# Kernel tuning notes

Measured on AMD Instinct MI355X. Metric: run time of the kernel, lower is better.

The kernel has to match this reference:

```python
import jax, jax.numpy as jnp
import numpy as np

B, T, I, H1, H2, OUT = 4096, 256, 2, 16, 64, 8


def _gru_layer(x, w_ih, w_hh, b_ih, b_hh):
    """PyTorch-semantics single-layer GRU. x: [T,B,I]. Returns (outputs [T,B,H], h_last [B,H]).
    Gate order is r,z,n as in torch.nn.GRU."""
    H = w_hh.shape[1]
    # precompute input projections for all timesteps (one big GEMM)
    gx_all = jnp.einsum('tbi,gi->tbg', x, w_ih) + b_ih  # [T,B,3H]

    def step(h, gx):
        gh = h @ w_hh.T + b_hh  # [B,3H]
        xr, xz, xn = jnp.split(gx, 3, axis=-1)
        hr, hz, hn = jnp.split(gh, 3, axis=-1)
        r = jax.nn.sigmoid(xr + hr)
        z = jax.nn.sigmoid(xz + hz)
        n = jnp.tanh(xn + r * hn)
        h_new = (1.0 - z) * n + z * h
        return h_new, h_new

    h0 = jnp.zeros((x.shape[1], H), dtype=x.dtype)
    h_last, out = jax.lax.scan(step, h0, gx_all)
    return out, h_last


def setup_inputs() -> dict:
    key = jax.random.key(0)
    ks = jax.random.split(key, 10)
    s = 0.3  # keep gates out of saturation, mimics orthogonal-ish scale
    return {
        'all_traj': jax.random.normal(ks[0], (B, T, I), jnp.float32),
        'w_ih1': s * jax.random.normal(ks[1], (3 * H1, I), jnp.float32),
        'w_hh1': s * jax.random.normal(ks[2], (3 * H1, H1), jnp.float32),
        'b_ih1': jnp.zeros((3 * H1,), jnp.float32),
        'b_hh1': jnp.zeros((3 * H1,), jnp.float32),
        'w_ih2f': s * jax.random.normal(ks[3], (3 * H2, H1), jnp.float32),
        'w_hh2f': s * jax.random.normal(ks[4], (3 * H2, H2), jnp.float32),
        'b_ih2f': jnp.zeros((3 * H2,), jnp.float32),
        'b_hh2f': jnp.zeros((3 * H2,), jnp.float32),
        'w_ih2b': s * jax.random.normal(ks[5], (3 * H2, H1), jnp.float32),
        'w_hh2b': s * jax.random.normal(ks[6], (3 * H2, H2), jnp.float32),
        'b_ih2b': jnp.zeros((3 * H2,), jnp.float32),
        'b_hh2b': jnp.zeros((3 * H2,), jnp.float32),
        'W1': 0.01 * jax.random.normal(ks[7], (32, H2), jnp.float32),
        'b1': jnp.zeros((32,), jnp.float32),
        'W2': 0.01 * jax.random.normal(ks[8], (OUT, 32), jnp.float32),
        'b2': jnp.zeros((OUT,), jnp.float32),
    }


def reference(all_traj, w_ih1, w_hh1, b_ih1, b_hh1,
              w_ih2f, w_hh2f, b_ih2f, b_hh2f,
              w_ih2b, w_hh2b, b_ih2b, b_hh2b,
              W1, b1, W2, b2):
    x = jnp.transpose(all_traj, (1, 0, 2))  # [T,B,I], matches torch.transpose(all_traj,0,1)
    out1, _ = _gru_layer(x, w_ih1, w_hh1, b_ih1, b_hh1)  # [T,B,16]
    # bidirectional layer: forward pass + reversed-time pass
    _, h_fwd = _gru_layer(out1, w_ih2f, w_hh2f, b_ih2f, b_hh2f)          # [B,64]
    _, h_bwd = _gru_layer(out1[::-1], w_ih2b, w_hh2b, b_ih2b, b_hh2b)    # [B,64]
    h = h_fwd + h_bwd  # torch.sum(h, 0) over the 2 directions -> [B,64]
    z = (h @ W1.T + b1) @ W2.T + b2  # MLP with no activation, as in source
    return z
```

## Files before the change

kernel.cpp:

```cpp
#include <hip/hip_runtime.h>

#define TT 256
#define BB 4096
#define EPB 4

__device__ __forceinline__ float sigm(float x) {
  float e = __expf(-x);
  return __builtin_amdgcn_rcpf(1.0f + e);
}

__device__ __forceinline__ float tanhx(float x) {
  x = fminf(15.0f, fmaxf(-15.0f, x));
  float e = __expf(-2.0f * x);
  return (1.0f - e) * __builtin_amdgcn_rcpf(1.0f + e);
}

#define DOT4(acc, wv, xv)                 \
  do {                                    \
    acc = fmaf((wv).x, (xv).x, acc);      \
    acc = fmaf((wv).y, (xv).y, acc);      \
    acc = fmaf((wv).z, (xv).z, acc);      \
    acc = fmaf((wv).w, (xv).w, acc);      \
  } while (0)

__global__ __launch_bounds__(128, 1) void gru_fused(
    const float* __restrict__ xin,
    const float* __restrict__ wih1,
    const float* __restrict__ whh1,
    const float* __restrict__ bih1,
    const float* __restrict__ bhh1,
    const float* __restrict__ wihf,
    const float* __restrict__ whhf,
    const float* __restrict__ bihf,
    const float* __restrict__ bhhf,
    const float* __restrict__ wihb,
    const float* __restrict__ whhb,
    const float* __restrict__ bihb,
    const float* __restrict__ bhhb,
    const float* __restrict__ W1,
    const float* __restrict__ b1,
    const float* __restrict__ W2,
    const float* __restrict__ b2,
    float* __restrict__ zout)
{
  __shared__ __align__(16) float out1L[EPB][TT][16];
  __shared__ __align__(16) float hs[2][EPB][64];
  __shared__ __align__(16) float hl1[EPB][16];
  __shared__ __align__(16) float ys[EPB][32];

  const int tid = threadIdx.x;
  const int w   = tid >> 6;
  const int l   = tid & 63;
  const int b0  = blockIdx.x * EPB;

  if (l < 32) {
    const int g = l >> 4;
    const int u = l & 15;
    const int e = w * 2 + g;

    float wr[16], wz[16], wn[16];
#pragma unroll
    for (int j = 0; j < 16; ++j) {
      wr[j] = whh1[u * 16 + j];
      wz[j] = whh1[(16 + u) * 16 + j];
      wn[j] = whh1[(32 + u) * 16 + j];
    }
    const float wir0 = wih1[2 * u],        wir1 = wih1[2 * u + 1];
    const float wiz0 = wih1[2 * (16 + u)], wiz1 = wih1[2 * (16 + u) + 1];
    const float win0 = wih1[2 * (32 + u)], win1 = wih1[2 * (32 + u) + 1];
    const float br  = bih1[u] + bhh1[u];
    const float bz  = bih1[16 + u] + bhh1[16 + u];
    const float bin = bih1[32 + u];
    const float bhn = bhh1[32 + u];

    const float2* xp = (const float2*)xin + (size_t)(b0 + e) * TT;

    float h = 0.0f;
    hl1[e][u] = 0.0f;
    for (int t = 0; t < TT; ++t) {
      float2 xv = xp[t];
      float ar = fmaf(wir1, xv.y, fmaf(wir0, xv.x, br));
      float az = fmaf(wiz1, xv.y, fmaf(wiz0, xv.x, bz));
      float an = fmaf(win1, xv.y, fmaf(win0, xv.x, bin));
      float hr = 0.f, hz = 0.f, hn = bhn;
#pragma unroll
      for (int j = 0; j < 16; ++j) {
        float hj = hl1[e][j];
        hr = fmaf(wr[j], hj, hr);
        hz = fmaf(wz[j], hj, hz);
        hn = fmaf(wn[j], hj, hn);
      }
      float r = sigm(ar + hr);
      float z = sigm(az + hz);
      float n = tanhx(fmaf(r, hn, an));
      h = fmaf(z, h - n, n);
      hl1[e][u] = h;
      out1L[e][t][u] = h;
    }
  }
  __syncthreads();

  const float* wih = w ? wihb : wihf;
  const float* whh = w ? whhb : whhf;
  const float* bih = w ? bihb : bihf;
  const float* bhh = w ? bhhb : bhhf;

  float4 wr2[16], wz2[16], wn2[16];
  {
    const float4* whh4 = (const float4*)whh;
#pragma unroll
    for (int j4 = 0; j4 < 16; ++j4) {
      wr2[j4] = whh4[l * 16 + j4];
      wz2[j4] = whh4[(64 + l) * 16 + j4];
      wn2[j4] = whh4[(128 + l) * 16 + j4];
    }
  }
  float4 wir2[4], wiz2[4], win2[4];
  {
    const float4* wih4 = (const float4*)wih;
#pragma unroll
    for (int i4 = 0; i4 < 4; ++i4) {
      wir2[i4] = wih4[l * 4 + i4];
      wiz2[i4] = wih4[(64 + l) * 4 + i4];
      win2[i4] = wih4[(128 + l) * 4 + i4];
    }
  }
  const float br2  = bih[l] + bhh[l];
  const float bz2  = bih[64 + l] + bhh[64 + l];
  const float bin2 = bih[128 + l];
  const float bhn2 = bhh[128 + l];

  float h0 = 0.f, h1 = 0.f, h2 = 0.f, h3 = 0.f;
  hs[w][0][l] = 0.f; hs[w][1][l] = 0.f; hs[w][2][l] = 0.f; hs[w][3][l] = 0.f;

#pragma unroll 1
  for (int t = 0; t < TT; ++t) {
    const int te = w ? (TT - 1 - t) : t;
    const float4* x0p = (const float4*)&out1L[0][te][0];
    const float4* x1p = (const float4*)&out1L[1][te][0];
    const float4* x2p = (const float4*)&out1L[2][te][0];
    const float4* x3p = (const float4*)&out1L[3][te][0];

    float ar0 = br2, az0 = bz2, an0 = bin2;
    float ar1 = br2, az1 = bz2, an1 = bin2;
    float ar2 = br2, az2 = bz2, an2 = bin2;
    float ar3 = br2, az3 = bz2, an3 = bin2;
#pragma unroll
    for (int i4 = 0; i4 < 4; ++i4) {
      const float4 wrv = wir2[i4], wzv = wiz2[i4], wnv = win2[i4];
      const float4 xa = x0p[i4], xb = x1p[i4], xc = x2p[i4], xd = x3p[i4];
      DOT4(ar0, wrv, xa); DOT4(az0, wzv, xa); DOT4(an0, wnv, xa);
      DOT4(ar1, wrv, xb); DOT4(az1, wzv, xb); DOT4(an1, wnv, xb);
      DOT4(ar2, wrv, xc); DOT4(az2, wzv, xc); DOT4(an2, wnv, xc);
      DOT4(ar3, wrv, xd); DOT4(az3, wzv, xd); DOT4(an3, wnv, xd);
    }

    float hr0 = 0.f, hz0 = 0.f, hn0 = bhn2;
    float hr1 = 0.f, hz1 = 0.f, hn1 = bhn2;
    float hr2 = 0.f, hz2 = 0.f, hn2 = bhn2;
    float hr3 = 0.f, hz3 = 0.f, hn3 = bhn2;
#pragma unroll
    for (int j4 = 0; j4 < 16; ++j4) {
      const float4 ha = *(const float4*)&hs[w][0][j4 * 4];
      const float4 hb = *(const float4*)&hs[w][1][j4 * 4];
      const float4 hc = *(const float4*)&hs[w][2][j4 * 4];
      const float4 hd = *(const float4*)&hs[w][3][j4 * 4];
      const float4 wrv = wr2[j4], wzv = wz2[j4], wnv = wn2[j4];
      DOT4(hr0, wrv, ha); DOT4(hz0, wzv, ha); DOT4(hn0, wnv, ha);
      DOT4(hr1, wrv, hb); DOT4(hz1, wzv, hb); DOT4(hn1, wnv, hb);
      DOT4(hr2, wrv, hc); DOT4(hz2, wzv, hc); DOT4(hn2, wnv, hc);
      DOT4(hr3, wrv, hd); DOT4(hz3, wzv, hd); DOT4(hn3, wnv, hd);
    }

    { float r = sigm(ar0 + hr0), z = sigm(az0 + hz0);
      float n = tanhx(fmaf(r, hn0, an0)); h0 = fmaf(z, h0 - n, n); }
    { float r = sigm(ar1 + hr1), z = sigm(az1 + hz1);
      float n = tanhx(fmaf(r, hn1, an1)); h1 = fmaf(z, h1 - n, n); }
    { float r = sigm(ar2 + hr2), z = sigm(az2 + hz2);
      float n = tanhx(fmaf(r, hn2, an2)); h2 = fmaf(z, h2 - n, n); }
    { float r = sigm(ar3 + hr3), z = sigm(az3 + hz3);
      float n = tanhx(fmaf(r, hn3, an3)); h3 = fmaf(z, h3 - n, n); }

    hs[w][0][l] = h0; hs[w][1][l] = h1; hs[w][2][l] = h2; hs[w][3][l] = h3;
  }
  __syncthreads();

  const int e3 = w * 2 + (l >> 5);
  const int s  = l & 31;
  const int bo = b0 + e3;
  {
    float acc = b1[s];
    const float4* w1r = (const float4*)(W1 + s * 64);
#pragma unroll
    for (int j4 = 0; j4 < 16; ++j4) {
      const float4 hv0 = *(const float4*)&hs[0][e3][j4 * 4];
      const float4 hv1 = *(const float4*)&hs[1][e3][j4 * 4];
      const float4 wv  = w1r[j4];
      acc = fmaf(wv.x, hv0.x + hv1.x, acc);
      acc = fmaf(wv.y, hv0.y + hv1.y, acc);
      acc = fmaf(wv.z, hv0.z + hv1.z, acc);
      acc = fmaf(wv.w, hv0.w + hv1.w, acc);
    }
    ys[e3][s] = acc;
  }
  if (s < 8) {
    float acc = b2[s];
#pragma unroll
    for (int j4 = 0; j4 < 8; ++j4) {
      const float4 yv = *(const float4*)&ys[e3][j4 * 4];
      const float4 wv = *(const float4*)&W2[s * 32 + j4 * 4];
      DOT4(acc, wv, yv);
    }
    zout[bo * 8 + s] = acc;
  }
}

extern "C" void kernel_launch(void* const* d_in, const int* in_sizes, int n_in,
                              void* d_out, int out_size, void* d_ws, size_t ws_size,
                              hipStream_t stream) {
  const float* all_traj = (const float*)d_in[0];
  const float* w_ih1  = (const float*)d_in[1];
  const float* w_hh1  = (const float*)d_in[2];
  const float* b_ih1  = (const float*)d_in[3];
  const float* b_hh1  = (const float*)d_in[4];
  const float* w_ih2f = (const float*)d_in[5];
  const float* w_hh2f = (const float*)d_in[6];
  const float* b_ih2f = (const float*)d_in[7];
  const float* b_hh2f = (const float*)d_in[8];
  const float* w_ih2b = (const float*)d_in[9];
  const float* w_hh2b = (const float*)d_in[10];
  const float* b_ih2b = (const float*)d_in[11];
  const float* b_hh2b = (const float*)d_in[12];
  const float* W1 = (const float*)d_in[13];
  const float* b1 = (const float*)d_in[14];
  const float* W2 = (const float*)d_in[15];
  const float* b2 = (const float*)d_in[16];
  float* z = (float*)d_out;

  gru_fused<<<BB / EPB, 128, 0, stream>>>(
      all_traj, w_ih1, w_hh1, b_ih1, b_hh1,
      w_ih2f, w_hh2f, b_ih2f, b_hh2f,
      w_ih2b, w_hh2b, b_ih2b, b_hh2b,
      W1, b1, W2, b2, z);
}
```

Before: 1.455 ms.

## Assign one batch element per wave per direction in bidirectional GRU layer

```diff
diff --git a/kernel.cpp b/kernel.cpp
--- a/kernel.cpp
+++ b/kernel.cpp
@@ -2,7 +2,7 @@
 
 #define TT 256
 #define BB 4096
-#define EPB 4
+#define EPB 2
 
 __device__ __forceinline__ float sigm(float x) {
   float e = __expf(-x);
@@ -23,7 +23,7 @@
     acc = fmaf((wv).w, (xv).w, acc);      \
   } while (0)
 
-__global__ __launch_bounds__(128, 1) void gru_fused(
+__global__ __launch_bounds__(256, 2) void gru_fused(
     const float* __restrict__ xin,
     const float* __restrict__ wih1,
     const float* __restrict__ whh1,
@@ -44,19 +44,20 @@
     float* __restrict__ zout)
 {
   __shared__ __align__(16) float out1L[EPB][TT][16];
-  __shared__ __align__(16) float hs[2][EPB][64];
+  __shared__ __align__(16) float hs[4][64];
   __shared__ __align__(16) float hl1[EPB][16];
   __shared__ __align__(16) float ys[EPB][32];
 
   const int tid = threadIdx.x;
   const int w   = tid >> 6;
   const int l   = tid & 63;
+  const int dir = w >> 1;
+  const int e   = w & 1;
   const int b0  = blockIdx.x * EPB;
 
-  if (l < 32) {
-    const int g = l >> 4;
-    const int u = l & 15;
-    const int e = w * 2 + g;
+  if (w < 2 && l < 16) {
+    const int u  = l;
+    const int e1 = w;
 
     float wr[16], wz[16], wn[16];
 #pragma unroll
@@ -73,10 +74,10 @@
     const float bin = bih1[32 + u];
     const float bhn = bhh1[32 + u];
 
-    const float2* xp = (const float2*)xin + (size_t)(b0 + e) * TT;
+    const float2* xp = (const float2*)xin + (size_t)(b0 + e1) * TT;
 
     float h = 0.0f;
-    hl1[e][u] = 0.0f;
+    hl1[e1][u] = 0.0f;
     for (int t = 0; t < TT; ++t) {
       float2 xv = xp[t];
       float ar = fmaf(wir1, xv.y, fmaf(wir0, xv.x, br));
@@ -85,7 +86,7 @@
       float hr = 0.f, hz = 0.f, hn = bhn;
 #pragma unroll
       for (int j = 0; j < 16; ++j) {
-        float hj = hl1[e][j];
+        float hj = hl1[e1][j];
         hr = fmaf(wr[j], hj, hr);
         hz = fmaf(wz[j], hj, hz);
         hn = fmaf(wn[j], hj, hn);
@@ -94,16 +95,16 @@
       float z = sigm(az + hz);
       float n = tanhx(fmaf(r, hn, an));
       h = fmaf(z, h - n, n);
-      hl1[e][u] = h;
-      out1L[e][t][u] = h;
+      hl1[e1][u] = h;
+      out1L[e1][t][u] = h;
     }
   }
   __syncthreads();
 
-  const float* wih = w ? wihb : wihf;
-  const float* whh = w ? whhb : whhf;
-  const float* bih = w ? bihb : bihf;
-  const float* bhh = w ? bhhb : bhhf;
+  const float* wih = dir ? wihb : wihf;
+  const float* whh = dir ? whhb : whhf;
+  const float* bih = dir ? bihb : bihf;
+  const float* bhh = dir ? bhhb : bhhf;
 
   float4 wr2[16], wz2[16], wn2[16];
   {
@@ -115,103 +116,90 @@
       wn2[j4] = whh4[(128 + l) * 16 + j4];
     }
   }
-  float4 wir2[4], wiz2[4], win2[4];
-  {
-    const float4* wih4 = (const float4*)wih;
-#pragma unroll
-    for (int i4 = 0; i4 < 4; ++i4) {
-      wir2[i4] = wih4[l * 4 + i4];
-      wiz2[i4] = wih4[(64 + l) * 4 + i4];
-      win2[i4] = wih4[(128 + l) * 4 + i4];
-    }
-  }
   const float br2  = bih[l] + bhh[l];
   const float bz2  = bih[64 + l] + bhh[64 + l];
   const float bin2 = bih[128 + l];
   const float bhn2 = bhh[128 + l];
 
-  float h0 = 0.f, h1 = 0.f, h2 = 0.f, h3 = 0.f;
-  hs[w][0][l] = 0.f; hs[w][1][l] = 0.f; hs[w][2][l] = 0.f; hs[w][3][l] = 0.f;
-
-#pragma unroll 1
-  for (int t = 0; t < TT; ++t) {
-    const int te = w ? (TT - 1 - t) : t;
-    const float4* x0p = (const float4*)&out1L[0][te][0];
-    const float4* x1p = (const float4*)&out1L[1][te][0];
-    const float4* x2p = (const float4*)&out1L[2][te][0];
-    const float4* x3p = (const float4*)&out1L[3][te][0];
-
-    float ar0 = br2, az0 = bz2, an0 = bin2;
-    float ar1 = br2, az1 = bz2, an1 = bin2;
-    float ar2 = br2, az2 = bz2, an2 = bin2;
-    float ar3 = br2, az3 = bz2, an3 = bin2;
+  float h = 0.f;
+  hs[w][l] = 0.f;
+
+  const float4* wp = (const float4*)wih;
+
+  for (int t2 = 0; t2 < TT / 2; ++t2) {
+    asm volatile("" : "+v"(wp));
+    const int ta = dir ? (TT - 1 - 2 * t2) : (2 * t2);
+    const int tb = dir ? (ta - 1) : (ta + 1);
+    const float4* xap = (const float4*)&out1L[e][ta][0];
+    const float4* xbp = (const float4*)&out1L[e][tb][0];
+
+    float arA = br2, azA = bz2, anA = bin2;
+    float arB = br2, azB = bz2, anB = bin2;
 #pragma unroll
     for (int i4 = 0; i4 < 4; ++i4) {
-      const float4 wrv = wir2[i4], wzv = wiz2[i4], wnv = win2[i4];
-      const float4 xa = x0p[i4], xb = x1p[i4], xc = x2p[i4], xd = x3p[i4];
-      DOT4(ar0, wrv, xa); DOT4(az0, wzv, xa); DOT4(an0, wnv, xa);
-      DOT4(ar1, wrv, xb); DOT4(az1, wzv, xb); DOT4(an1, wnv, xb);
-      DOT4(ar2, wrv, xc); DOT4(az2, wzv, xc); DOT4(an2, wnv, xc);
-      DOT4(ar3, wrv, xd); DOT4(az3, wzv, xd); DOT4(an3, wnv, xd);
-    }
-
-    float hr0 = 0.f, hz0 = 0.f, hn0 = bhn2;
-    float hr1 = 0.f, hz1 = 0.f, hn1 = bhn2;
-    float hr2 = 0.f, hz2 = 0.f, hn2 = bhn2;
-    float hr3 = 0.f, hz3 = 0.f, hn3 = bhn2;
-#pragma unroll
-    for (int j4 = 0; j4 < 16; ++j4) {
-      const float4 ha = *(const float4*)&hs[w][0][j4 * 4];
-      const float4 hb = *(const float4*)&hs[w][1][j4 * 4];
-      const float4 hc = *(const float4*)&hs[w][2][j4 * 4];
-      const float4 hd = *(const float4*)&hs[w][3][j4 * 4];
-      const float4 wrv = wr2[j4], wzv = wz2[j4], wnv = wn2[j4];
-      DOT4(hr0, wrv, ha); DOT4(hz0, wzv, ha); DOT4(hn0, wnv, ha);
-      DOT4(hr1, wrv, hb); DOT4(hz1, wzv, hb); DOT4(hn1, wnv, hb);
-      DOT4(hr2, wrv, hc); DOT4(hz2, wzv, hc); DOT4(hn2, wnv, hc);
-      DOT4(hr3, wrv, hd); DOT4(hz3, wzv, hd); DOT4(hn3, wnv, hd);
-    }
-
-    { float r = sigm(ar0 + hr0), z = sigm(az0 + hz0);
-      float n = tanhx(fmaf(r, hn0, an0)); h0 = fmaf(z, h0 - n, n); }
-    { float r = sigm(ar1 + hr1), z = sigm(az1 + hz1);
-      float n = tanhx(fmaf(r, hn1, an1)); h1 = fmaf(z, h1 - n, n); }
-    { float r = sigm(ar2 + hr2), z = sigm(az2 + hz2);
-      float n = tanhx(fmaf(r, hn2, an2)); h2 = fmaf(z, h2 - n, n); }
-    { float r = sigm(ar3 + hr3), z = sigm(az3 + hz3);
-      float n = tanhx(fmaf(r, hn3, an3)); h3 = fmaf(z, h3 - n, n); }
-
-    hs[w][0][l] = h0; hs[w][1][l] = h1; hs[w][2][l] = h2; hs[w][3][l] = h3;
+      const float4 wrv = wp[l * 4 + i4];
+      const float4 wzv = wp[(64 + l) * 4 + i4];
+      const float4 wnv = wp[(128 + l) * 4 + i4];
+      const float4 va = xap[i4];
+      const float4 vb = xbp[i4];
+      DOT4(arA, wrv, va); DOT4(azA, wzv, va); DOT4(anA, wnv, va);
+      DOT4(arB, wrv, vb); DOT4(azB, wzv, vb); DOT4(anB, wnv, vb);
+    }
+
+    {
+      float hr = 0.f, hz = 0.f, hn = bhn2;
+#pragma unroll
+      for (int j4 = 0; j4 < 16; ++j4) {
+        const float4 hv = *(const float4*)&hs[w][j4 * 4];
+        DOT4(hr, wr2[j4], hv); DOT4(hz, wz2[j4], hv); DOT4(hn, wn2[j4], hv);
+      }
+      float r = sigm(arA + hr);
+      float z = sigm(azA + hz);
+      float n = tanhx(fmaf(r, hn, anA));
+      h = fmaf(z, h - n, n);
+      hs[w][l] = h;
+    }
+    {
+      float hr = 0.f, hz = 0.f, hn = bhn2;
+#pragma unroll
+      for (int j4 = 0; j4 < 16; ++j4) {
+        const float4 hv = *(const float4*)&hs[w][j4 * 4];
+        DOT4(hr, wr2[j4], hv); DOT4(hz, wz2[j4], hv); DOT4(hn, wn2[j4], hv);
+      }
+      float r = sigm(arB + hr);
+      float z = sigm(azB + hz);
+      float n = tanhx(fmaf(r, hn, anB));
+      h = fmaf(z, h - n, n);
+      hs[w][l] = h;
+    }
   }
   __syncthreads();
 
-  const int e3 = w * 2 + (l >> 5);
-  const int s  = l & 31;
-  const int bo = b0 + e3;
-  {
+  if (w < 2 && l < 32) {
+    const int s = l;
     float acc = b1[s];
     const float4* w1r = (const float4*)(W1 + s * 64);
 #pragma unroll
     for (int j4 = 0; j4 < 16; ++j4) {
-      const float4 hv0 = *(const float4*)&hs[0][e3][j4 * 4];
-      const float4 hv1 = *(const float4*)&hs[1][e3][j4 * 4];
+      const float4 hv0 = *(const float4*)&hs[w][j4 * 4];
+      const float4 hv1 = *(const float4*)&hs[2 + w][j4 * 4];
       const float4 wv  = w1r[j4];
       acc = fmaf(wv.x, hv0.x + hv1.x, acc);
       acc = fmaf(wv.y, hv0.y + hv1.y, acc);
       acc = fmaf(wv.z, hv0.z + hv1.z, acc);
       acc = fmaf(wv.w, hv0.w + hv1.w, acc);
     }
-    ys[e3][s] = acc;
-  }
-  if (s < 8) {
-    float acc = b2[s];
+    ys[w][s] = acc;
+  }
+  if (w < 2 && l < 8) {
+    float acc = b2[l];
 #pragma unroll
     for (int j4 = 0; j4 < 8; ++j4) {
-      const float4 yv = *(const float4*)&ys[e3][j4 * 4];
-      const float4 wv = *(const float4*)&W2[s * 32 + j4 * 4];
+      const float4 yv = *(const float4*)&ys[w][j4 * 4];
+      const float4 wv = *(const float4*)&W2[l * 32 + j4 * 4];
       DOT4(acc, wv, yv);
     }
-    zout[bo * 8 + s] = acc;
+    zout[(b0 + w) * 8 + l] = acc;
   }
 }
 
@@ -237,7 +225,7 @@
   const float* b2 = (const float*)d_in[16];
   float* z = (float*)d_out;
 
-  gru_fused<<<BB / EPB, 128, 0, stream>>>(
+  gru_fused<<<BB / EPB, 256, 0, stream>>>(
       all_traj, w_ih1, w_hh1, b_ih1, b_hh1,
       w_ih2f, w_hh2f, b_ih2f, b_hh2f,
       w_ih2b, w_hh2b, b_ih2b, b_hh2b,
```

New measurement: 2.436 ms. 1.67x slower.
